# Kernel optimization log

Measured on AMD Instinct MI355X. Metric: run time of the kernel, lower is better.

## Reference

```python
import jax, jax.numpy as jnp
import numpy as np
from jax import lax

# Norse default LIF/LI parameters with dt=0.001
DT_TAU_MEM = 0.1   # dt * tau_mem_inv (1/1e-2)
DT_TAU_SYN = 0.2   # dt * tau_syn_inv (1/5e-3)
V_TH = 0.5
ALPHA = 100.0      # SuperSpike surrogate slope (backward only)

@jax.custom_vjp
def spike(x):
    return (x > 0).astype(x.dtype)

def _spike_fwd(x):
    return (x > 0).astype(x.dtype), x

def _spike_bwd(x, g):
    # SuperSpike surrogate gradient: 1 / (alpha*|x| + 1)^2
    sg = 1.0 / (ALPHA * jnp.abs(x) + 1.0) ** 2
    return (g * sg,)

spike.defvjp(_spike_fwd, _spike_bwd)

def setup_inputs() -> dict:
    key = jax.random.key(0)
    k1, k2, k3 = jax.random.split(key, 3)
    T, B, C, H, W = 64, 512, 1, 28, 28
    IN, HID, OUT = 784, 2048, 10
    x = jax.random.normal(k1, (T, B, C, H, W), dtype=jnp.float32)
    # Kaiming-uniform-ish bias-free Linear weights, torch layout [out, in]
    w1 = jax.random.uniform(k2, (HID, IN), jnp.float32, -1.0, 1.0) / np.sqrt(IN)
    w_out = jax.random.uniform(k3, (OUT, HID), jnp.float32, -1.0, 1.0) / np.sqrt(HID)
    return {"x": x, "w1": w1, "w_out": w_out}

def reference(x, w1, w_out):
    T, B = x.shape[0], x.shape[1]
    HID, OUT = w1.shape[0], w_out.shape[0]
    xf = x.reshape(T, B, -1)  # [T, B, IN]

    def step(carry, xt):
        v1, i1, vo, io = carry
        cur = xt @ w1.T                       # fc1: [B, HID]
        # LIF: decay, threshold/spike/reset, then integrate new input current
        v1_dec = v1 + DT_TAU_MEM * (-v1 + i1)
        i1_dec = i1 * (1.0 - DT_TAU_SYN)
        z = spike(v1_dec - V_TH)
        v1_new = (1.0 - z) * v1_dec           # v_reset = 0
        i1_new = i1_dec + cur
        out_cur = z @ w_out.T                 # fc_out: [B, OUT]
        # LI readout: leaky integration (no spiking)
        vo_new = vo + DT_TAU_MEM * (-vo + io)
        io_new = io * (1.0 - DT_TAU_SYN) + out_cur
        return (v1_new, i1_new, vo_new, io_new), vo_new

    zh = jnp.zeros((B, HID), x.dtype)
    zo = jnp.zeros((B, OUT), x.dtype)
    _, voltages = lax.scan(step, (zh, zh, zo, zo), xf)  # [T, B, OUT]
    return jnp.max(voltages, axis=0)
```

## Files before the change

### kernel.cpp

```cpp
#include <hip/hip_runtime.h>
#include <cstdint>
#include <cstddef>

#define T_STEPS 64
#define BATCH 512
#define IN_F 784
#define NKT 25
#define HID 2048
#define OUT_F 10

#define DEC_V 0.9f
#define DEC_I 0.8f
#define DT_V 0.1f
#define V_TH 0.5f

typedef __attribute__((ext_vector_type(8))) _Float16 f16x8;
typedef __attribute__((ext_vector_type(4))) float f32x4;

__device__ __forceinline__ void load_lds16h(const _Float16* g, _Float16* l) {
  __builtin_amdgcn_global_load_lds(
      (const __attribute__((address_space(1))) void*)g,
      (__attribute__((address_space(3))) void*)l, 16, 0, 0);
}

__global__ __launch_bounds__(256)
void split_frag(const float* __restrict__ src, _Float16* __restrict__ hiT,
                _Float16* __restrict__ loT) {
  __shared__ float xr[16][804];
  const int mt = blockIdx.x;
  for (int i = threadIdx.x; i < 16 * IN_F; i += 256) {
    const int r = i / IN_F, c = i - r * IN_F;
    xr[r][c] = src[(size_t)(mt * 16 + r) * IN_F + c];
  }
  for (int i = threadIdx.x; i < 16 * 16; i += 256)
    xr[i >> 4][IN_F + (i & 15)] = 0.0f;
  __syncthreads();

  const int l = threadIdx.x & 63;
  const int g = threadIdx.x >> 6;
  const int r = l & 15, q = l >> 4;
  for (int kt = g; kt < NKT; kt += 4) {
    const float* s = &xr[r][kt * 32 + q * 8];
    f16x8 h, lo;
#pragma unroll
    for (int j = 0; j < 8; ++j) {
      const float v = s[j];
      const _Float16 hh = (_Float16)v;
      h[j] = hh;
      lo[j] = (_Float16)(v - (float)hh);
    }
    const size_t off = ((size_t)mt * NKT + kt) * 512 + l * 8;
    *(f16x8*)&hiT[off] = h;
    *(f16x8*)&loT[off] = lo;
  }
}

__global__ __launch_bounds__(256, 2)
void gemm_fc1(const _Float16* __restrict__ AhT, const _Float16* __restrict__ AlT,
              const _Float16* __restrict__ WhT, const _Float16* __restrict__ WlT,
              float* __restrict__ C) {
  __shared__ _Float16 __attribute__((aligned(16))) sAh[2][8 * 512];
  __shared__ _Float16 __attribute__((aligned(16))) sAl[2][8 * 512];

  const int tid = threadIdx.x;
  const int lane = tid & 63;
  const int wv = tid >> 6;

  const int nwg = gridDim.x * gridDim.y;
  const int bid = blockIdx.y * gridDim.x + blockIdx.x;
  const int q = nwg >> 3;
  const int swz = (bid & 7) * q + (bid >> 3);
  const int bx = swz & 7;
  const int by = swz >> 3;

  const int bmT = by * 8;
  const int bnT = bx * 16;

  const int wrT = (wv >> 1) * 4;
  const int wcT = (wv & 1) * 8;
  const int col = lane & 15;
  const int quad = lane >> 4;

  f32x4 acc[4][8] = {};

#pragma unroll
  for (int j = 0; j < 2; ++j) {
    const int t = wv * 2 + j;
    const size_t go = ((size_t)(bmT + t) * NKT + 0) * 512 + lane * 8;
    load_lds16h(AhT + go, &sAh[0][t * 512]);
    load_lds16h(AlT + go, &sAl[0][t * 512]);
  }
  __syncthreads();

  for (int kt = 0; kt < NKT; ++kt) {
    const int cur = kt & 1;
    if (kt + 1 < NKT) {
#pragma unroll
      for (int j = 0; j < 2; ++j) {
        const int t = wv * 2 + j;
        const size_t go = ((size_t)(bmT + t) * NKT + (kt + 1)) * 512 + lane * 8;
        load_lds16h(AhT + go, &sAh[cur ^ 1][t * 512]);
        load_lds16h(AlT + go, &sAl[cur ^ 1][t * 512]);
      }
    }

    f16x8 fah[4], fal[4];
#pragma unroll
    for (int i = 0; i < 4; ++i) {
      fah[i] = *(const f16x8*)&sAh[cur][(wrT + i) * 512 + lane * 8];
      fal[i] = *(const f16x8*)&sAl[cur][(wrT + i) * 512 + lane * 8];
    }

    const size_t wbase = ((size_t)(bnT + wcT) * NKT + kt) * 512 + lane * 8;
#pragma unroll
    for (int ni = 0; ni < 8; ++ni) {
      const size_t wo = wbase + (size_t)ni * ((size_t)NKT * 512);
      const f16x8 fwh = *(const f16x8*)&WhT[wo];
      const f16x8 fwl = *(const f16x8*)&WlT[wo];
#pragma unroll
      for (int mi = 0; mi < 4; ++mi) {
        acc[mi][ni] = __builtin_amdgcn_mfma_f32_16x16x32_f16(fah[mi], fwh, acc[mi][ni], 0, 0, 0);
        acc[mi][ni] = __builtin_amdgcn_mfma_f32_16x16x32_f16(fah[mi], fwl, acc[mi][ni], 0, 0, 0);
        acc[mi][ni] = __builtin_amdgcn_mfma_f32_16x16x32_f16(fal[mi], fwh, acc[mi][ni], 0, 0, 0);
      }
    }
    __syncthreads();
  }

  const int rowb = by * 128 + (wv >> 1) * 64;
  const int colb = bx * 256 + (wv & 1) * 128;
#pragma unroll
  for (int mi = 0; mi < 4; ++mi)
#pragma unroll
    for (int ni = 0; ni < 8; ++ni)
#pragma unroll
      for (int r = 0; r < 4; ++r)
        C[(size_t)(rowb + mi * 16 + quad * 4 + r) * HID + colb + ni * 16 + col] =
            acc[mi][ni][r];
}

__global__ __launch_bounds__(256)
void lif_out(const float* __restrict__ cur, const float* __restrict__ wo,
             float* __restrict__ v1, float* __restrict__ i1,
             float* __restrict__ outP, int tc, int t0) {
  __shared__ _Float16 zL[T_STEPS][264];
  __shared__ _Float16 wT[16][264];

  const int tid = threadIdx.x;
  const int hc = blockIdx.x;
  const int b = blockIdx.y;
  const int hb = hc * 256;

  for (int i = tid; i < 16 * 256; i += 256) {
    const int n = i >> 8, k = i & 255;
    wT[n][k] = (n < OUT_F) ? (_Float16)wo[(size_t)n * HID + hb + k] : (_Float16)0.f;
  }

  const int sidx = b * HID + hb + tid;
  float v = v1[sidx];
  float ci = i1[sidx];
#pragma unroll 4
  for (int t = 0; t < tc; ++t) {
    const float c = cur[(size_t)t * (BATCH * HID) + sidx];
    const float vd = DEC_V * v + DT_V * ci;
    const float z = (vd > V_TH) ? 1.0f : 0.0f;
    v = (1.0f - z) * vd;
    ci = DEC_I * ci + c;
    zL[t][tid] = (_Float16)z;
  }
  v1[sidx] = v;
  i1[sidx] = ci;
  __syncthreads();

  const int wv = tid >> 6;
  const int lane = tid & 63;
  const int col = lane & 15;
  const int quad = lane >> 4;
  f32x4 acc = {};
  const _Float16* za = &zL[wv * 16 + col][0];
  const _Float16* wb = &wT[col][0];
#pragma unroll
  for (int ks = 0; ks < 8; ++ks) {
    f16x8 a = *(const f16x8*)(za + ks * 32 + quad * 8);
    f16x8 bb = *(const f16x8*)(wb + ks * 32 + quad * 8);
    acc = __builtin_amdgcn_mfma_f32_16x16x32_f16(a, bb, acc, 0, 0, 0);
  }
  if (col < OUT_F) {
#pragma unroll
    for (int r = 0; r < 4; ++r) {
      const int t = wv * 16 + quad * 4 + r;
      if (t < tc)
        outP[(((size_t)hc * T_STEPS + (t0 + t)) * BATCH + b) * OUT_F + col] = acc[r];
    }
  }
}

__global__ __launch_bounds__(256)
void li_scan(const float* __restrict__ outP, float* __restrict__ out) {
  const int idx = blockIdx.x * 256 + threadIdx.x;
  if (idx >= BATCH * OUT_F) return;
  float vo = 0.f, io = 0.f, vmax = 0.f;
  for (int t = 0; t < T_STEPS; ++t) {
    float oc = 0.f;
#pragma unroll
    for (int hc = 0; hc < 8; ++hc)
      oc += outP[((size_t)hc * T_STEPS + t) * (BATCH * OUT_F) + idx];
    const float von = DEC_V * vo + DT_V * io;
    io = DEC_I * io + oc;
    vo = von;
    vmax = fmaxf(vmax, von);
  }
  out[idx] = vmax;
}

__global__ void zero_state(float* __restrict__ p, int n) {
  int i = blockIdx.x * 256 + threadIdx.x;
  if (i < n) p[i] = 0.0f;
}

extern "C" void kernel_launch(void* const* d_in, const int* in_sizes, int n_in,
                              void* d_out, int out_size, void* d_ws, size_t ws_size,
                              hipStream_t stream) {
  const float* x  = (const float*)d_in[0];
  const float* w1 = (const float*)d_in[1];
  const float* wo = (const float*)d_in[2];
  float* out = (float*)d_out;

  const size_t BH = (size_t)BATCH * HID;
  const size_t WT_HALVES = (size_t)(HID / 16) * NKT * 512;

  float* v1 = (float*)d_ws;
  float* i1 = v1 + BH;
  float* outP = i1 + BH;
  _Float16* WhT = (_Float16*)(outP + (size_t)8 * T_STEPS * BATCH * OUT_F);
  _Float16* WlT = WhT + WT_HALVES;
  char* chunk0 = (char*)(WlT + WT_HALVES);

  const size_t base_bytes = (size_t)(chunk0 - (char*)d_ws);
  const size_t per_step = BH * 4 + (size_t)2 * 32 * NKT * 512 * 2;
  int Tc = T_STEPS;
  while (Tc > 1 && base_bytes + (size_t)Tc * per_step > ws_size) Tc >>= 1;

  float* cur = (float*)chunk0;
  _Float16* AhT = (_Float16*)(cur + (size_t)Tc * BH);
  _Float16* AlT = AhT + (size_t)Tc * 32 * NKT * 512;

  split_frag<<<HID / 16, 256, 0, stream>>>(w1, WhT, WlT);
  zero_state<<<(int)((2 * BH + 255) / 256), 256, 0, stream>>>(v1, (int)(2 * BH));

  for (int t0 = 0; t0 < T_STEPS; t0 += Tc) {
    const int tc = (T_STEPS - t0 < Tc) ? (T_STEPS - t0) : Tc;
    const int nrows = tc * BATCH;
    split_frag<<<nrows / 16, 256, 0, stream>>>(x + (size_t)t0 * BATCH * IN_F, AhT, AlT);
    dim3 grid(HID / 256, nrows / 128);
    gemm_fc1<<<grid, 256, 0, stream>>>(AhT, AlT, WhT, WlT, cur);
    dim3 lgrid(HID / 256, BATCH);
    lif_out<<<lgrid, 256, 0, stream>>>(cur, wo, v1, i1, outP, tc, t0);
  }
  li_scan<<<(BATCH * OUT_F + 255) / 256, 256, 0, stream>>>(outP, out);
}
```

Baseline: 679.1 us.

## Stage W fragments through LDS and enlarge fc1 GEMM tile to 256x256

The fc1 GEMM now uses 512-thread workgroups with a 256x256 output tile, and loads both the A and W hi/lo fragments into double-buffered LDS through global_load_lds. Before, each wave read its W fragments straight from global memory. The aim is to cut repeated global reads of W and halve the number of row blocks. In exchange, LDS use grows to 128 KB per block, which limits occupancy, and fewer workgroups are launched.

```diff
diff --git a/kernel.cpp b/kernel.cpp
--- a/kernel.cpp
+++ b/kernel.cpp
@@ -55,12 +55,14 @@
   }
 }
 
-__global__ __launch_bounds__(256, 2)
+__global__ __launch_bounds__(512, 2)
 void gemm_fc1(const _Float16* __restrict__ AhT, const _Float16* __restrict__ AlT,
               const _Float16* __restrict__ WhT, const _Float16* __restrict__ WlT,
               float* __restrict__ C) {
-  __shared__ _Float16 __attribute__((aligned(16))) sAh[2][8 * 512];
-  __shared__ _Float16 __attribute__((aligned(16))) sAl[2][8 * 512];
+  __shared__ _Float16 __attribute__((aligned(16))) sAh[2][16 * 512];
+  __shared__ _Float16 __attribute__((aligned(16))) sAl[2][16 * 512];
+  __shared__ _Float16 __attribute__((aligned(16))) sWh[2][16 * 512];
+  __shared__ _Float16 __attribute__((aligned(16))) sWl[2][16 * 512];
 
   const int tid = threadIdx.x;
   const int lane = tid & 63;
@@ -73,70 +75,68 @@
   const int bx = swz & 7;
   const int by = swz >> 3;
 
-  const int bmT = by * 8;
+  const int bmT = by * 16;
   const int bnT = bx * 16;
 
-  const int wrT = (wv >> 1) * 4;
-  const int wcT = (wv & 1) * 8;
+  const int wr = wv >> 2;
+  const int wc = wv & 3;
   const int col = lane & 15;
   const int quad = lane >> 4;
 
-  f32x4 acc[4][8] = {};
-
-#pragma unroll
-  for (int j = 0; j < 2; ++j) {
-    const int t = wv * 2 + j;
-    const size_t go = ((size_t)(bmT + t) * NKT + 0) * 512 + lane * 8;
-    load_lds16h(AhT + go, &sAh[0][t * 512]);
-    load_lds16h(AlT + go, &sAl[0][t * 512]);
-  }
+  f32x4 acc[8][4] = {};
+
+#define STAGE(KT, BUF)                                                       \
+  do {                                                                       \
+    _Pragma("unroll")                                                        \
+    for (int j = 0; j < 2; ++j) {                                            \
+      const int t = wv * 2 + j;                                              \
+      const size_t ga = ((size_t)(bmT + t) * NKT + (KT)) * 512 + lane * 8;   \
+      load_lds16h(AhT + ga, &sAh[BUF][t * 512]);                             \
+      load_lds16h(AlT + ga, &sAl[BUF][t * 512]);                             \
+      const size_t gw = ((size_t)(bnT + t) * NKT + (KT)) * 512 + lane * 8;   \
+      load_lds16h(WhT + gw, &sWh[BUF][t * 512]);                             \
+      load_lds16h(WlT + gw, &sWl[BUF][t * 512]);                             \
+    }                                                                        \
+  } while (0)
+
+  STAGE(0, 0);
   __syncthreads();
 
   for (int kt = 0; kt < NKT; ++kt) {
     const int cur = kt & 1;
-    if (kt + 1 < NKT) {
-#pragma unroll
-      for (int j = 0; j < 2; ++j) {
-        const int t = wv * 2 + j;
-        const size_t go = ((size_t)(bmT + t) * NKT + (kt + 1)) * 512 + lane * 8;
-        load_lds16h(AhT + go, &sAh[cur ^ 1][t * 512]);
-        load_lds16h(AlT + go, &sAl[cur ^ 1][t * 512]);
+    if (kt + 1 < NKT) STAGE(kt + 1, cur ^ 1);
+
+    f16x8 fah[8], fal[8];
+#pragma unroll
+    for (int i = 0; i < 8; ++i) {
+      fah[i] = *(const f16x8*)&sAh[cur][(wr * 8 + i) * 512 + lane * 8];
+      fal[i] = *(const f16x8*)&sAl[cur][(wr * 8 + i) * 512 + lane * 8];
+    }
+#pragma unroll
+    for (int nj = 0; nj < 4; ++nj) {
+      const f16x8 fwh = *(const f16x8*)&sWh[cur][(wc * 4 + nj) * 512 + lane * 8];
+      const f16x8 fwl = *(const f16x8*)&sWl[cur][(wc * 4 + nj) * 512 + lane * 8];
+#pragma unroll
+      for (int mi = 0; mi < 8; ++mi) {
+        acc[mi][nj] = __builtin_amdgcn_mfma_f32_16x16x32_f16(fah[mi], fwh, acc[mi][nj], 0, 0, 0);
+        acc[mi][nj] = __builtin_amdgcn_mfma_f32_16x16x32_f16(fah[mi], fwl, acc[mi][nj], 0, 0, 0);
+        acc[mi][nj] = __builtin_amdgcn_mfma_f32_16x16x32_f16(fal[mi], fwh, acc[mi][nj], 0, 0, 0);
       }
     }
-
-    f16x8 fah[4], fal[4];
-#pragma unroll
-    for (int i = 0; i < 4; ++i) {
-      fah[i] = *(const f16x8*)&sAh[cur][(wrT + i) * 512 + lane * 8];
-      fal[i] = *(const f16x8*)&sAl[cur][(wrT + i) * 512 + lane * 8];
-    }
-
-    const size_t wbase = ((size_t)(bnT + wcT) * NKT + kt) * 512 + lane * 8;
-#pragma unroll
-    for (int ni = 0; ni < 8; ++ni) {
-      const size_t wo = wbase + (size_t)ni * ((size_t)NKT * 512);
-      const f16x8 fwh = *(const f16x8*)&WhT[wo];
-      const f16x8 fwl = *(const f16x8*)&WlT[wo];
-#pragma unroll
-      for (int mi = 0; mi < 4; ++mi) {
-        acc[mi][ni] = __builtin_amdgcn_mfma_f32_16x16x32_f16(fah[mi], fwh, acc[mi][ni], 0, 0, 0);
-        acc[mi][ni] = __builtin_amdgcn_mfma_f32_16x16x32_f16(fah[mi], fwl, acc[mi][ni], 0, 0, 0);
-        acc[mi][ni] = __builtin_amdgcn_mfma_f32_16x16x32_f16(fal[mi], fwh, acc[mi][ni], 0, 0, 0);
-      }
-    }
     __syncthreads();
   }
-
-  const int rowb = by * 128 + (wv >> 1) * 64;
-  const int colb = bx * 256 + (wv & 1) * 128;
-#pragma unroll
-  for (int mi = 0; mi < 4; ++mi)
-#pragma unroll
-    for (int ni = 0; ni < 8; ++ni)
+#undef STAGE
+
+  const int rowb = by * 256 + wr * 128;
+  const int colb = bx * 256 + wc * 64;
+#pragma unroll
+  for (int mi = 0; mi < 8; ++mi)
+#pragma unroll
+    for (int nj = 0; nj < 4; ++nj)
 #pragma unroll
       for (int r = 0; r < 4; ++r)
-        C[(size_t)(rowb + mi * 16 + quad * 4 + r) * HID + colb + ni * 16 + col] =
-            acc[mi][ni][r];
+        C[(size_t)(rowb + mi * 16 + quad * 4 + r) * HID + colb + nj * 16 + col] =
+            acc[mi][nj][r];
 }
 
 __global__ __launch_bounds__(256)
@@ -252,8 +252,8 @@
     const int tc = (T_STEPS - t0 < Tc) ? (T_STEPS - t0) : Tc;
     const int nrows = tc * BATCH;
     split_frag<<<nrows / 16, 256, 0, stream>>>(x + (size_t)t0 * BATCH * IN_F, AhT, AlT);
-    dim3 grid(HID / 256, nrows / 128);
-    gemm_fc1<<<grid, 256, 0, stream>>>(AhT, AlT, WhT, WlT, cur);
+    dim3 grid(HID / 256, nrows / 256);
+    gemm_fc1<<<grid, 512, 0, stream>>>(AhT, AlT, WhT, WlT, cur);
     dim3 lgrid(HID / 256, BATCH);
     lif_out<<<lgrid, 256, 0, stream>>>(cur, wo, v1, i1, outP, tc, t0);
   }
```

Result: faster. 636.8 us (-6.2%).
